# Kernel tuning notes

Hardware: AMD Instinct MI355X
Metric: run time of the kernel (lower is better)

The kernel has to match this reference:

```python
import jax, jax.numpy as jnp
import numpy as np

N, E = 20000, 640000
LATENT, HID, OUT, HEADS = 512, 256, 128, 2
NEG_SLOPE = 0.2


def setup_inputs() -> dict:
    key = jax.random.key(0)
    ks = jax.random.split(key, 12)
    s = 0.02
    return {
        "z": jax.random.normal(ks[0], (N, LATENT), dtype=jnp.float32),
        "edge_index": jax.random.randint(ks[1], (2, E), 0, N, dtype=jnp.int64),
        "W1": jax.random.normal(ks[2], (LATENT, HID), dtype=jnp.float32) * s,
        "b1": jnp.zeros((HID,), dtype=jnp.float32),
        "W2": jax.random.normal(ks[3], (HID, HID * HEADS), dtype=jnp.float32) * s,
        "b2": jnp.zeros((HID * HEADS,), dtype=jnp.float32),
        "Wg": jax.random.normal(ks[4], (HID * HEADS, HEADS * OUT), dtype=jnp.float32) * s,
        "att_src": jax.random.normal(ks[5], (HEADS, OUT), dtype=jnp.float32) * s,
        "att_dst": jax.random.normal(ks[6], (HEADS, OUT), dtype=jnp.float32) * s,
        "bias_g": jnp.zeros((HEADS * OUT,), dtype=jnp.float32),
        "W3": jax.random.normal(ks[7], (OUT * HEADS, 512), dtype=jnp.float32) * s,
        "b3": jnp.zeros((512,), dtype=jnp.float32),
    }


def _gat_conv(x, edge_index, Wg, att_src, att_dst, bias_g):
    n = x.shape[0]
    # add self loops (PyG GATConv default add_self_loops=True)
    loops = jnp.tile(jnp.arange(n, dtype=edge_index.dtype)[None, :], (2, 1))
    ei = jnp.concatenate([edge_index, loops], axis=1)
    src, dst = ei[0], ei[1]
    xp = (x @ Wg).reshape(n, HEADS, OUT)          # [N,H,C]
    a_src = jnp.einsum('nhc,hc->nh', xp, att_src)  # [N,H]
    a_dst = jnp.einsum('nhc,hc->nh', xp, att_dst)
    alpha = jax.nn.leaky_relu(a_src[src] + a_dst[dst], NEG_SLOPE)  # [E+N,H]
    amax = jax.ops.segment_max(alpha, dst, num_segments=n)
    alpha = jnp.exp(alpha - amax[dst])
    denom = jax.ops.segment_sum(alpha, dst, num_segments=n)
    alpha = alpha / jnp.maximum(denom[dst], 1e-16)
    msg = xp[src] * alpha[:, :, None]              # [E+N,H,C]
    out = jax.ops.segment_sum(msg, dst, num_segments=n)  # [N,H,C]
    return out.reshape(n, HEADS * OUT) + bias_g


def reference(z, edge_index, W1, b1, W2, b2, Wg, att_src, att_dst, bias_g, W3, b3):
    x = jax.nn.relu(z @ W1 + b1)
    x = jax.nn.relu(x @ W2 + b2)
    x = _gat_conv(x, edge_index, Wg, att_src, att_dst, bias_g)
    return x @ W3 + b3
```

## Files before the change

### kernel.cpp

```cpp
#include <hip/hip_runtime.h>
#include <hip/hip_bf16.h>
#include <float.h>

#define N_NODES 20000
#define LATENT  512
#define HID     256
#define OUT_C   128
#define HEADS   2
#define HC      256
#define NEG_SLOPE 0.2f

typedef _Float16 half8 __attribute__((ext_vector_type(8)));
typedef __attribute__((ext_vector_type(4))) float f32x4;
typedef __attribute__((ext_vector_type(2))) float f32x2;

__device__ __forceinline__ ushort f2h(float v) {
    _Float16 h = (_Float16)v;
    return *(ushort*)&h;
}
__device__ __forceinline__ float h2f(ushort u) {
    _Float16 h = *(_Float16*)&u;
    return (float)h;
}

#if __has_builtin(__builtin_amdgcn_cvt_pk_fp8_f32) && __has_builtin(__builtin_amdgcn_cvt_pk_f32_fp8)
#define FP8_HW 1
#else
#define FP8_HW 0
#endif

__device__ __forceinline__ uint f32_to_e4m3(float v) {
#if FP8_HW
    return (uint)(__builtin_amdgcn_cvt_pk_fp8_f32(v, v, 0, false) & 0xff);
#else
    _Float16 hf = (_Float16)(v * 0.00390625f);
    uint hb = *(ushort*)&hf;
    uint s = (hb >> 8) & 0x80;
    uint mag = hb & 0x7fff;
    mag = (mag + 0x3f + ((mag >> 7) & 1)) >> 7;
    if (mag > 0x7e) mag = 0x7e;
    return s | mag;
#endif
}

__device__ __forceinline__ void gl_lds16(const ushort* g, ushort* l) {
    __builtin_amdgcn_global_load_lds(
        (const __attribute__((address_space(1))) unsigned int*)g,
        (__attribute__((address_space(3))) unsigned int*)l, 16, 0, 0);
}

__global__ __launch_bounds__(512) void fused_mlp(
    const ushort* __restrict__ z16, const ushort* __restrict__ W1T,
    const float* __restrict__ b1, const ushort* __restrict__ W2T,
    const float* __restrict__ b2, const ushort* __restrict__ WgT,
    const float* __restrict__ attS, const float* __restrict__ attD,
    float* __restrict__ aS, float* __restrict__ aD,
    unsigned char* __restrict__ xp8, int M)
{
    __shared__ ushort lds[65536];

    const int t = threadIdx.x;
    const int l = t & 63;
    const int w = t >> 6;
    const int wr = w & 3;
    const int wc = w >> 2;
    const int lm = l & 15;
    const int q  = l >> 4;
    const int q4 = q * 4;
    const int row0 = (int)blockIdx.x * 64;
    const int lr16 = l >> 2;
    const int gsh = (((l & 3) ^ ((l >> 4) & 3)) << 3);
    const int csw = ((q ^ ((lm >> 2) & 3)) << 3);

    constexpr int X1 = 0;
    constexpr int X2 = 16384;
    constexpr int SB = 49152;

    auto p1b = [&](int c) { int b = c % 3; return b == 0 ? SB : b == 1 ? X2 : X2 + 10240; };
    auto p2b = [&](int c) { int b = c % 3; return b == 0 ? SB : b == 1 ? X2 : X2 + 16384; };
    auto p3b = [&](int c) { int b = c % 3; return b == 0 ? SB : b == 1 ? SB + 8192 : X1; };

    auto issue1 = [&](int c) {
        ushort* B = &lds[p1b(c)];
        const int kk = c * 32;
        #pragma unroll
        for (int u = 0; u < 3; ++u) {
            const int ii = w + u * 8;
            if (ii < 20) {
                const ushort* g = (ii < 4)
                    ? z16 + (size_t)(row0 + ii * 16 + lr16) * 512 + kk + gsh
                    : W1T + (size_t)((ii - 4) * 16 + lr16) * 512 + kk + gsh;
                gl_lds16(g, B + ii * 512);
            }
        }
    };
    auto issue2 = [&](int c) {
        ushort* B = &lds[p2b(c)];
        const int kk = c * 32;
        #pragma unroll
        for (int u = 0; u < 4; ++u) {
            const int ii = w + u * 8;
            gl_lds16(W2T + (size_t)(ii * 16 + lr16) * 256 + kk + gsh, B + ii * 512);
        }
    };
    auto issue3 = [&](int c) {
        ushort* B = &lds[p3b(c)];
        const int kk = c * 32;
        #pragma unroll
        for (int u = 0; u < 2; ++u) {
            const int ii = w + u * 8;
            gl_lds16(WgT + (size_t)(ii * 16 + lr16) * 512 + kk + gsh, B + ii * 512);
        }
    };

    auto wait3i = [&](int c, int NC) {
        __builtin_amdgcn_sched_barrier(0);
        if (c + 1 < NC) {
            if (w < 4) asm volatile("s_waitcnt vmcnt(3)" ::: "memory");
            else       asm volatile("s_waitcnt vmcnt(2)" ::: "memory");
        } else         asm volatile("s_waitcnt vmcnt(0)" ::: "memory");
        __builtin_amdgcn_s_barrier();
        __builtin_amdgcn_sched_barrier(0);
    };
    auto wait4 = [&](int c, int NC) {
        __builtin_amdgcn_sched_barrier(0);
        if (c + 1 < NC) asm volatile("s_waitcnt vmcnt(4)" ::: "memory");
        else            asm volatile("s_waitcnt vmcnt(0)" ::: "memory");
        __builtin_amdgcn_s_barrier();
        __builtin_amdgcn_sched_barrier(0);
    };
    auto wait2 = [&](int c, int NC) {
        __builtin_amdgcn_sched_barrier(0);
        if (c + 1 < NC) asm volatile("s_waitcnt vmcnt(2)" ::: "memory");
        else            asm volatile("s_waitcnt vmcnt(0)" ::: "memory");
        __builtin_amdgcn_s_barrier();
        __builtin_amdgcn_sched_barrier(0);
    };

    const f32x4 zf = {0.f, 0.f, 0.f, 0.f};

    f32x4 acc1[8];
    #pragma unroll
    for (int i = 0; i < 8; ++i) acc1[i] = zf;

    issue1(0); issue1(1);
    for (int c = 0; c < 16; ++c) {
        wait3i(c, 16);
        if (c + 2 < 16) issue1(c + 2);
        const ushort* B = &lds[p1b(c)];
        half8 af = *(const half8*)&B[(wr * 16 + lm) * 32 + csw];
        #pragma unroll
        for (int ni = 0; ni < 8; ++ni) {
            half8 bf = *(const half8*)&B[2048 + (wc * 128 + ni * 16 + lm) * 32 + csw];
            acc1[ni] = __builtin_amdgcn_mfma_f32_16x16x32_f16(af, bf, acc1[ni], 0, 0, 0);
        }
    }
    __builtin_amdgcn_s_barrier();
    issue2(0); issue2(1);
    #pragma unroll
    for (int ni = 0; ni < 8; ++ni) {
        const int col = wc * 128 + ni * 16 + lm;
        const float bv = b1[col];
        const int ch = col >> 5, c5 = col & 31;
        #pragma unroll
        for (int r = 0; r < 4; ++r) {
            const int row = wr * 16 + q4 + r;
            const float v = fmaxf(acc1[ni][r] + bv, 0.f);
            lds[X1 + ch * 2048 + row * 32 + (((c5 >> 3) ^ q) << 3) + (c5 & 7)] = f2h(v);
        }
    }
    asm volatile("s_waitcnt lgkmcnt(0)" ::: "memory");
    __builtin_amdgcn_s_barrier();
    __builtin_amdgcn_sched_barrier(0);

    f32x4 acc2[16];
    #pragma unroll
    for (int i = 0; i < 16; ++i) acc2[i] = zf;

    for (int c = 0; c < 8; ++c) {
        wait4(c, 8);
        if (c + 2 < 8) issue2(c + 2);
        const ushort* B = &lds[p2b(c)];
        half8 af = *(const half8*)&lds[X1 + c * 2048 + (wr * 16 + lm) * 32 + csw];
        #pragma unroll
        for (int ni = 0; ni < 16; ++ni) {
            half8 bf = *(const half8*)&B[(wc * 256 + ni * 16 + lm) * 32 + csw];
            acc2[ni] = __builtin_amdgcn_mfma_f32_16x16x32_f16(af, bf, acc2[ni], 0, 0, 0);
        }
    }
    __builtin_amdgcn_s_barrier();
    issue3(0); issue3(1);
    #pragma unroll
    for (int ni = 0; ni < 16; ++ni) {
        const int col = wc * 256 + ni * 16 + lm;
        const float bv = b2[col];
        const int ch = col >> 5, c5 = col & 31;
        #pragma unroll
        for (int r = 0; r < 4; ++r) {
            const int row = wr * 16 + q4 + r;
            const float v = fmaxf(acc2[ni][r] + bv, 0.f);
            lds[X2 + ch * 2048 + row * 32 + (((c5 >> 3) ^ q) << 3) + (c5 & 7)] = f2h(v);
        }
    }
    asm volatile("s_waitcnt lgkmcnt(0)" ::: "memory");
    __builtin_amdgcn_s_barrier();
    __builtin_amdgcn_sched_barrier(0);

    f32x4 acc3[8];
    #pragma unroll
    for (int i = 0; i < 8; ++i) acc3[i] = zf;

    for (int c = 0; c < 16; ++c) {
        wait2(c, 16);
        if (c + 2 < 16) issue3(c + 2);
        const ushort* B = &lds[p3b(c)];
        half8 af = *(const half8*)&lds[X2 + c * 2048 + (wr * 16 + lm) * 32 + csw];
        #pragma unroll
        for (int ni = 0; ni < 8; ++ni) {
            half8 bf = *(const half8*)&B[(wc * 128 + ni * 16 + lm) * 32 + csw];
            acc3[ni] = __builtin_amdgcn_mfma_f32_16x16x32_f16(af, bf, acc3[ni], 0, 0, 0);
        }
    }

    const int h = wc;
    float asv[8], adv[8];
    #pragma unroll
    for (int ni = 0; ni < 8; ++ni) {
        const int col = wc * 128 + ni * 16 + lm;
        asv[ni] = attS[col];
        adv[ni] = attD[col];
    }
    #pragma unroll
    for (int r = 0; r < 4; ++r) {
        const int row = row0 + wr * 16 + q4 + r;
        float ps = 0.f, pd = 0.f;
        #pragma unroll
        for (int ni = 0; ni < 8; ++ni) {
            const float v = acc3[ni][r];
            ps += v * asv[ni];
            pd += v * adv[ni];
            if (row < M)
                xp8[(size_t)row * HC + wc * 128 + ni * 16 + lm] =
                    (unsigned char)f32_to_e4m3(v);
        }
        #pragma unroll
        for (int off = 8; off > 0; off >>= 1) {
            ps += __shfl_xor(ps, off);
            pd += __shfl_xor(pd, off);
        }
        if (lm == 0 && row < M) {
            atomicAdd(&aS[2 * row + h], ps);
            atomicAdd(&aD[2 * row + h], pd);
        }
    }
}

template<int BN, int LOGNBY>
__global__ __launch_bounds__(256, 4) void gemm_f16(
    const ushort* __restrict__ A, const ushort* __restrict__ BT,
    const float* __restrict__ bias,
    float* __restrict__ Cf, ushort* __restrict__ Ch,
    int M, int N, int K, int relu)
{
    static_assert(BN == 64, "vmcnt immediates assume 3 DMAs/chunk");
    constexpr int NI  = BN / 32;
    constexpr int BUF = 4096 + BN * 32;
    __shared__ ushort lds[3 * BUF];

    const int t = threadIdx.x;
    const int l = t & 63;
    const int w = t >> 6;
    const int wm = (w >> 1) * 64;
    const int wn = (w & 1) * (BN / 2);
    const int lm = l & 15;
    const int q  = l >> 4;
    const int q4 = q * 4;

    const int T  = (int)gridDim.x;
    const int qq = T >> 3, rr = T & 7;
    const int kx = (int)blockIdx.x & 7;
    const int jx = (int)blockIdx.x >> 3;
    const int lin = kx * qq + (kx < rr ? kx : rr) + jx;
    const int row0 = (lin >> LOGNBY) * 128;
    const int col0 = (lin & ((1 << LOGNBY) - 1)) * BN;

    const int jr0 = w * 16 + (l >> 2);
    const int gsh = (((l & 3) ^ ((l >> 4) & 3)) << 3);
    const ushort* gA0 = A + (size_t)(row0 + jr0) * K + gsh;
    const ushort* gA1 = gA0 + (size_t)64 * K;
    const ushort* gB0 = BT + (size_t)(col0 + jr0) * K + gsh;
    const int dA0 = w * 512, dA1 = (4 + w) * 512;
    const int dB0 = 4096 + w * 512;

    const int csw = ((q ^ ((lm >> 2) & 3)) << 3);

    const f32x4 zf = {0.f, 0.f, 0.f, 0.f};
    f32x4 acc[4][NI];
    #pragma unroll
    for (int i = 0; i < 4; ++i)
        #pragma unroll
        for (int j = 0; j < NI; ++j) acc[i][j] = zf;

    const int NC = K >> 5;

    auto issue = [&](int c) {
        ushort* B = lds + (size_t)(c % 3) * BUF;
        const int kk = c * 32;
        gl_lds16(gA0 + kk, B + dA0);
        gl_lds16(gA1 + kk, B + dA1);
        gl_lds16(gB0 + kk, B + dB0);
    };

    auto compute = [&](int c) {
        const ushort* B = lds + (size_t)(c % 3) * BUF;
        half8 bf[NI];
        #pragma unroll
        for (int ni = 0; ni < NI; ++ni) {
            const int boff = (wn + ni * 16 + lm) * 32 + csw;
            bf[ni] = *(const half8*)&B[4096 + boff];
        }
        #pragma unroll
        for (int mi = 0; mi < 4; ++mi) {
            const int aoff = (wm + mi * 16 + lm) * 32 + csw;
            half8 af = *(const half8*)&B[aoff];
            #pragma unroll
            for (int ni = 0; ni < NI; ++ni)
                acc[mi][ni] = __builtin_amdgcn_mfma_f32_16x16x32_f16(
                    af, bf[ni], acc[mi][ni], 0, 0, 0);
        }
    };

    issue(0); issue(1);
    for (int c = 0; c < NC; ++c) {
        __builtin_amdgcn_sched_barrier(0);
        if (c + 1 < NC) asm volatile("s_waitcnt vmcnt(3)" ::: "memory");
        else            asm volatile("s_waitcnt vmcnt(0)" ::: "memory");
        __builtin_amdgcn_s_barrier();
        __builtin_amdgcn_sched_barrier(0);
        if (c + 2 < NC) issue(c + 2);
        compute(c);
    }

    #pragma unroll
    for (int mi = 0; mi < 4; ++mi) {
        #pragma unroll
        for (int ni = 0; ni < NI; ++ni) {
            const int col = col0 + wn + ni * 16 + lm;
            const float bv = bias ? bias[col] : 0.f;
            #pragma unroll
            for (int r = 0; r < 4; ++r) {
                const int row = row0 + wm + mi * 16 + q4 + r;
                if (row >= M) continue;
                float v = acc[mi][ni][r] + bv;
                if (relu) v = fmaxf(v, 0.f);
                const size_t idx = (size_t)row * N + col;
                if (Cf) Cf[idx] = v;
                if (Ch) Ch[idx] = f2h(v);
            }
        }
    }
}

#define CVT_BLOCKS 10000
#define TR_BLOCKS  2048
__global__ __launch_bounds__(256) void prologue_kernel(
    const float* __restrict__ z, ushort* __restrict__ z_f16,
    int* deg, int* cursor, float* aS, float* aD, int n,
    const float* __restrict__ W1, const float* __restrict__ W2,
    const float* __restrict__ Wg, const float* __restrict__ W3,
    ushort* __restrict__ T1, ushort* __restrict__ T2,
    ushort* __restrict__ Tg, ushort* __restrict__ T3)
{
    const int b = blockIdx.x;
    if (b < CVT_BLOCKS) {
        int i = b * 256 + threadIdx.x;
        if (i < n) {
            deg[i] = 0; cursor[i] = 0;
            ((float2*)aS)[i] = make_float2(0.f, 0.f);
            ((float2*)aD)[i] = make_float2(0.f, 0.f);
        }
        float4 v = ((const float4*)z)[i];
        ((ushort4*)z_f16)[i] = make_ushort4(f2h(v.x), f2h(v.y), f2h(v.z), f2h(v.w));
    } else {
        int idx = (b - CVT_BLOCKS) * 256 + threadIdx.x;
        int which = idx >> 17, i = idx & 131071;
        const float* W; ushort* T; int K, N;
        if (which == 0)      { W = W1; T = T1; K = 512; N = 256; }
        else if (which == 1) { W = W2; T = T2; K = 256; N = 512; }
        else if (which == 2) { W = Wg; T = Tg; K = 512; N = 256; }
        else                 { W = W3; T = T3; K = 256; N = 512; }
        int k = i / N, nn = i - k * N;
        T[(size_t)nn * K + k] = f2h(W[i]);
    }
}

__global__ __launch_bounds__(256) void hist_kernel(
    const int* __restrict__ dst, int* deg, int E_real, int ET)
{
    int e = blockIdx.x * blockDim.x + threadIdx.x;
    if (e >= ET) return;
    int d = (e < E_real) ? dst[e] : (e - E_real);
    atomicAdd(&deg[d], 1);
}

__global__ __launch_bounds__(1024) void scan_kernel(
    const int* __restrict__ deg, int* __restrict__ rowptr, int n)
{
    __shared__ int part[1024];
    const int t = threadIdx.x;
    const int chunk = (n + 1023) / 1024;
    const int lo = t * chunk;
    const int hi = min(lo + chunk, n);
    int s = 0;
    for (int i = lo; i < hi; ++i) s += deg[i];
    part[t] = s;
    __syncthreads();
    #pragma unroll
    for (int off = 1; off < 1024; off <<= 1) {
        int add = (t >= off) ? part[t - off] : 0;
        __syncthreads();
        part[t] += add;
        __syncthreads();
    }
    int run = part[t] - s;
    for (int i = lo; i < hi; ++i) { rowptr[i] = run; run += deg[i]; }
    if (t == 1023) rowptr[n] = part[1023];
}

__global__ __launch_bounds__(256) void scatter_kernel(
    const int* __restrict__ src, const int* __restrict__ dst,
    const int* __restrict__ rowptr, int* cursor,
    int* __restrict__ sorted_src, int E_real, int ET)
{
    int e = blockIdx.x * blockDim.x + threadIdx.x;
    if (e >= ET) return;
    int s, d;
    if (e < E_real) { s = src[e]; d = dst[e]; }
    else            { s = e - E_real; d = s; }
    int pos = rowptr[d] + atomicAdd(&cursor[d], 1);
    sorted_src[pos] = s;
}

__global__ __launch_bounds__(256) void gat_aggregate(
    const int* __restrict__ rowptr, const int* __restrict__ sorted_src,
    const float* __restrict__ a_src, const float* __restrict__ a_dst,
    const unsigned char* __restrict__ xp8, const float* __restrict__ bias_g,
    ushort* __restrict__ xg, int n)
{
    const int d = blockIdx.x * 4 + (threadIdx.x >> 6);
    if (d >= n) return;
    const int lane = threadIdx.x & 63;
    const int hsel = lane & 32;
    const int start = rowptr[d], end = rowptr[d + 1];

    const float ad0 = a_dst[2 * d + 0];
    const float ad1 = a_dst[2 * d + 1];

    float4 acc = make_float4(0.f, 0.f, 0.f, 0.f);
    float denom = 0.f;

    for (int e0 = start; e0 < end; e0 += 32) {
        const int cnt = min(32, end - e0);
        const int idx = lane & 31;
        float wsel = 0.f; int off = 0;
        if (idx < cnt) {
            int s = sorted_src[e0 + idx];
            float v0 = a_src[2 * s + 0] + ad0;
            float v1 = a_src[2 * s + 1] + ad1;
            v0 = (v0 > 0.f) ? v0 : NEG_SLOPE * v0;
            v1 = (v1 > 0.f) ? v1 : NEG_SLOPE * v1;
            wsel = (lane < 32) ? __expf(v0) : __expf(v1);
            off = s * HC;
        }
        int j = 0;
        for (; j + 8 <= cnt; j += 8) {
            float w_[8]; int o_[8];
            #pragma unroll
            for (int u = 0; u < 8; ++u) {
                w_[u] = __shfl(wsel, (j + u) + hsel);
                o_[u] = __shfl(off, j + u);
            }
            uint v_[8];
            #pragma unroll
            for (int u = 0; u < 8; ++u)
                v_[u] = *(const uint*)(xp8 + o_[u] + 4 * lane);
            #pragma unroll
            for (int u = 0; u < 8; ++u) {
                denom += w_[u];
#if FP8_HW
                f32x2 lo = __builtin_amdgcn_cvt_pk_f32_fp8((int)v_[u], false);
                f32x2 hi = __builtin_amdgcn_cvt_pk_f32_fp8((int)v_[u], true);
                acc.x += w_[u] * lo.x; acc.y += w_[u] * lo.y;
                acc.z += w_[u] * hi.x; acc.w += w_[u] * hi.y;
#else
                const float wu = w_[u] * 256.0f;
                const uint b = v_[u];
                acc.x += wu * h2f(((b & 0x80u) << 8) | ((b & 0x7fu) << 7));
                acc.y += wu * h2f((((b >> 8) & 0x80u) << 8) | (((b >> 8) & 0x7fu) << 7));
                acc.z += wu * h2f((((b >> 16) & 0x80u) << 8) | (((b >> 16) & 0x7fu) << 7));
                acc.w += wu * h2f((((b >> 24) & 0x80u) << 8) | (((b >> 24) & 0x7fu) << 7));
#endif
            }
        }
        for (; j < cnt; ++j) {
            const float w = __shfl(wsel, j + hsel);
            const int   o = __shfl(off, j);
            const uint  b = *(const uint*)(xp8 + o + 4 * lane);
            denom += w;
#if FP8_HW
            f32x2 lo = __builtin_amdgcn_cvt_pk_f32_fp8((int)b, false);
            f32x2 hi = __builtin_amdgcn_cvt_pk_f32_fp8((int)b, true);
            acc.x += w * lo.x; acc.y += w * lo.y;
            acc.z += w * hi.x; acc.w += w * hi.y;
#else
            const float wu = w * 256.0f;
            acc.x += wu * h2f(((b & 0x80u) << 8) | ((b & 0x7fu) << 7));
            acc.y += wu * h2f((((b >> 8) & 0x80u) << 8) | (((b >> 8) & 0x7fu) << 7));
            acc.z += wu * h2f((((b >> 16) & 0x80u) << 8) | (((b >> 16) & 0x7fu) << 7));
            acc.w += wu * h2f((((b >> 24) & 0x80u) << 8) | (((b >> 24) & 0x7fu) << 7));
#endif
        }
    }

    const float inv = 1.f / fmaxf(denom, 1e-16f);
    const int c = 4 * lane;
    const float4 bg = *(const float4*)(bias_g + c);
    const size_t base = ((size_t)d * HC + c) >> 2;
    ((ushort4*)xg)[base] = make_ushort4(
        f2h(acc.x * inv + bg.x), f2h(acc.y * inv + bg.y),
        f2h(acc.z * inv + bg.z), f2h(acc.w * inv + bg.w));
}

extern "C" void kernel_launch(void* const* d_in, const int* in_sizes, int n_in,
                              void* d_out, int out_size, void* d_ws, size_t ws_size,
                              hipStream_t stream)
{
    const float* z       = (const float*)d_in[0];
    const int*   ei      = (const int*)d_in[1];
    const float* W1      = (const float*)d_in[2];
    const float* b1      = (const float*)d_in[3];
    const float* W2      = (const float*)d_in[4];
    const float* b2      = (const float*)d_in[5];
    const float* Wg      = (const float*)d_in[6];
    const float* att_src = (const float*)d_in[7];
    const float* att_dst = (const float*)d_in[8];
    const float* bias_g  = (const float*)d_in[9];
    const float* W3      = (const float*)d_in[10];
    const float* b3      = (const float*)d_in[11];
    float* out = (float*)d_out;

    const int n = N_NODES;
    const int E_real = in_sizes[1] / 2;
    const int ET = E_real + n;
    const int* src = ei;
    const int* dst = ei + E_real;

    char* p = (char*)d_ws;
    auto alloc = [&](size_t bytes) {
        char* r = p;
        p += (bytes + 63) & ~(size_t)63;
        return r;
    };
    const int np = n + 128;
    ushort* z_f16  = (ushort*)alloc((size_t)np * LATENT * 2);
    ushort* xg_f16 = (ushort*)alloc((size_t)np * HID * 2);
    unsigned char* xp8 = (unsigned char*)alloc((size_t)n * HC);
    ushort* W1T = (ushort*)alloc((size_t)LATENT * HID * 2);
    ushort* W2T = (ushort*)alloc((size_t)HID * 512 * 2);
    ushort* WgT = (ushort*)alloc((size_t)512 * HC * 2);
    ushort* W3T = (ushort*)alloc((size_t)HC * 512 * 2);
    float* a_src = (float*)alloc((size_t)2 * n * 4);
    float* a_dst = (float*)alloc((size_t)2 * n * 4);
    int* deg        = (int*)alloc((size_t)n * 4);
    int* rowptr     = (int*)alloc(((size_t)n + 1) * 4);
    int* cursor     = (int*)alloc((size_t)n * 4);
    int* sorted_src = (int*)alloc((size_t)ET * 4);

    const int gm128 = (n + 127) / 128;

    prologue_kernel<<<CVT_BLOCKS + TR_BLOCKS, 256, 0, stream>>>(
        z, z_f16, deg, cursor, a_src, a_dst, n,
        W1, W2, Wg, W3, W1T, W2T, WgT, W3T);
    hist_kernel<<<(ET + 255) / 256, 256, 0, stream>>>(dst, deg, E_real, ET);
    scan_kernel<<<1, 1024, 0, stream>>>(deg, rowptr, n);
    scatter_kernel<<<(ET + 255) / 256, 256, 0, stream>>>(
        src, dst, rowptr, cursor, sorted_src, E_real, ET);

    fused_mlp<<<(n + 63) / 64, 512, 0, stream>>>(
        z_f16, W1T, b1, W2T, b2, WgT,
        att_src, att_dst, a_src, a_dst, xp8, n);

    gat_aggregate<<<(n + 3) / 4, 256, 0, stream>>>(
        rowptr, sorted_src, a_src, a_dst, xp8, bias_g, xg_f16, n);

    gemm_f16<64, 3><<<gm128 * 8, 256, 0, stream>>>(
        xg_f16, W3T, b3, out, nullptr, n, 512, HC, 0);
}
```

Measured before the change: 296.5 us.

## Slab-stream layer-2 output into layer-3 GEMM to cut LDS and registers

Restructures the fused MLP so the second GEMM is computed in four 128-column slabs, each immediately consumed by the Wg GEMM as a K-chunk, instead of materializing the full 512-wide hidden activation in LDS. This shrinks LDS from 128KB to 80KB and the layer-2 accumulators from 16 to 4 fragments, and adds a launch-bounds occupancy hint of 4. The aim is more resident blocks per CU and better latency hiding. In exchange it adds more barriers, smaller double-buffered loads, and finer-grained waitcnt scheduling, which raises the risk of pipeline stalls.

```diff
diff --git a/kernel.cpp b/kernel.cpp
--- a/kernel.cpp
+++ b/kernel.cpp
@@ -49,7 +49,7 @@
         (__attribute__((address_space(3))) unsigned int*)l, 16, 0, 0);
 }
 
-__global__ __launch_bounds__(512) void fused_mlp(
+__global__ __launch_bounds__(512, 4) void fused_mlp(
     const ushort* __restrict__ z16, const ushort* __restrict__ W1T,
     const float* __restrict__ b1, const ushort* __restrict__ W2T,
     const float* __restrict__ b2, const ushort* __restrict__ WgT,
@@ -57,7 +57,7 @@
     float* __restrict__ aS, float* __restrict__ aD,
     unsigned char* __restrict__ xp8, int M)
 {
-    __shared__ ushort lds[65536];
+    __shared__ ushort lds[40960];
 
     const int t = threadIdx.x;
     const int l = t & 63;
@@ -72,16 +72,17 @@
     const int gsh = (((l & 3) ^ ((l >> 4) & 3)) << 3);
     const int csw = ((q ^ ((lm >> 2) & 3)) << 3);
 
-    constexpr int X1 = 0;
-    constexpr int X2 = 16384;
-    constexpr int SB = 49152;
-
-    auto p1b = [&](int c) { int b = c % 3; return b == 0 ? SB : b == 1 ? X2 : X2 + 10240; };
-    auto p2b = [&](int c) { int b = c % 3; return b == 0 ? SB : b == 1 ? X2 : X2 + 16384; };
-    auto p3b = [&](int c) { int b = c % 3; return b == 0 ? SB : b == 1 ? SB + 8192 : X1; };
+    constexpr int X1   = 0;
+    constexpr int SLAB = 16384;
+    constexpr int SB   = 24576;
+
+    auto barsync = [&]() {
+        __builtin_amdgcn_s_barrier();
+        __builtin_amdgcn_sched_barrier(0);
+    };
 
     auto issue1 = [&](int c) {
-        ushort* B = &lds[p1b(c)];
+        ushort* B = &lds[(c % 3) * 10240];
         const int kk = c * 32;
         #pragma unroll
         for (int u = 0; u < 3; ++u) {
@@ -94,60 +95,37 @@
             }
         }
     };
-    auto issue2 = [&](int c) {
-        ushort* B = &lds[p2b(c)];
-        const int kk = c * 32;
-        #pragma unroll
-        for (int u = 0; u < 4; ++u) {
-            const int ii = w + u * 8;
-            gl_lds16(W2T + (size_t)(ii * 16 + lr16) * 256 + kk + gsh, B + ii * 512);
-        }
-    };
-    auto issue3 = [&](int c) {
-        ushort* B = &lds[p3b(c)];
-        const int kk = c * 32;
+    auto issue2 = [&](int s, int c) {
+        ushort* B = &lds[SLAB + (c & 1) * 4096];
+        gl_lds16(W2T + (size_t)(s * 128 + w * 16 + lr16) * 256 + c * 32 + gsh,
+                 B + w * 512);
+    };
+    auto issue3 = [&](int s, int c) {
+        ushort* B = &lds[SB + (c & 1) * 8192];
         #pragma unroll
         for (int u = 0; u < 2; ++u) {
             const int ii = w + u * 8;
-            gl_lds16(WgT + (size_t)(ii * 16 + lr16) * 512 + kk + gsh, B + ii * 512);
-        }
-    };
-
-    auto wait3i = [&](int c, int NC) {
+            gl_lds16(WgT + (size_t)(ii * 16 + lr16) * 512 + s * 128 + c * 32 + gsh,
+                     B + ii * 512);
+        }
+    };
+
+    const f32x4 zf = {0.f, 0.f, 0.f, 0.f};
+
+    f32x4 acc1[8];
+    #pragma unroll
+    for (int i = 0; i < 8; ++i) acc1[i] = zf;
+
+    issue1(0); issue1(1);
+    for (int c = 0; c < 16; ++c) {
         __builtin_amdgcn_sched_barrier(0);
-        if (c + 1 < NC) {
+        if (c + 1 < 16) {
             if (w < 4) asm volatile("s_waitcnt vmcnt(3)" ::: "memory");
             else       asm volatile("s_waitcnt vmcnt(2)" ::: "memory");
         } else         asm volatile("s_waitcnt vmcnt(0)" ::: "memory");
-        __builtin_amdgcn_s_barrier();
-        __builtin_amdgcn_sched_barrier(0);
-    };
-    auto wait4 = [&](int c, int NC) {
-        __builtin_amdgcn_sched_barrier(0);
-        if (c + 1 < NC) asm volatile("s_waitcnt vmcnt(4)" ::: "memory");
-        else            asm volatile("s_waitcnt vmcnt(0)" ::: "memory");
-        __builtin_amdgcn_s_barrier();
-        __builtin_amdgcn_sched_barrier(0);
-    };
-    auto wait2 = [&](int c, int NC) {
-        __builtin_amdgcn_sched_barrier(0);
-        if (c + 1 < NC) asm volatile("s_waitcnt vmcnt(2)" ::: "memory");
-        else            asm volatile("s_waitcnt vmcnt(0)" ::: "memory");
-        __builtin_amdgcn_s_barrier();
-        __builtin_amdgcn_sched_barrier(0);
-    };
-
-    const f32x4 zf = {0.f, 0.f, 0.f, 0.f};
-
-    f32x4 acc1[8];
-    #pragma unroll
-    for (int i = 0; i < 8; ++i) acc1[i] = zf;
-
-    issue1(0); issue1(1);
-    for (int c = 0; c < 16; ++c) {
-        wait3i(c, 16);
+        barsync();
         if (c + 2 < 16) issue1(c + 2);
-        const ushort* B = &lds[p1b(c)];
+        const ushort* B = &lds[(c % 3) * 10240];
         half8 af = *(const half8*)&B[(wr * 16 + lm) * 32 + csw];
         #pragma unroll
         for (int ni = 0; ni < 8; ++ni) {
@@ -156,7 +134,7 @@
         }
     }
     __builtin_amdgcn_s_barrier();
-    issue2(0); issue2(1);
+    issue2(0, 0); issue2(0, 1);
     #pragma unroll
     for (int ni = 0; ni < 8; ++ni) {
         const int col = wc * 128 + ni * 16 + lm;
@@ -170,56 +148,68 @@
         }
     }
     asm volatile("s_waitcnt lgkmcnt(0)" ::: "memory");
-    __builtin_amdgcn_s_barrier();
-    __builtin_amdgcn_sched_barrier(0);
-
-    f32x4 acc2[16];
-    #pragma unroll
-    for (int i = 0; i < 16; ++i) acc2[i] = zf;
-
-    for (int c = 0; c < 8; ++c) {
-        wait4(c, 8);
-        if (c + 2 < 8) issue2(c + 2);
-        const ushort* B = &lds[p2b(c)];
-        half8 af = *(const half8*)&lds[X1 + c * 2048 + (wr * 16 + lm) * 32 + csw];
-        #pragma unroll
-        for (int ni = 0; ni < 16; ++ni) {
-            half8 bf = *(const half8*)&B[(wc * 256 + ni * 16 + lm) * 32 + csw];
-            acc2[ni] = __builtin_amdgcn_mfma_f32_16x16x32_f16(af, bf, acc2[ni], 0, 0, 0);
-        }
-    }
-    __builtin_amdgcn_s_barrier();
-    issue3(0); issue3(1);
-    #pragma unroll
-    for (int ni = 0; ni < 16; ++ni) {
-        const int col = wc * 256 + ni * 16 + lm;
-        const float bv = b2[col];
-        const int ch = col >> 5, c5 = col & 31;
-        #pragma unroll
-        for (int r = 0; r < 4; ++r) {
-            const int row = wr * 16 + q4 + r;
-            const float v = fmaxf(acc2[ni][r] + bv, 0.f);
-            lds[X2 + ch * 2048 + row * 32 + (((c5 >> 3) ^ q) << 3) + (c5 & 7)] = f2h(v);
-        }
-    }
-    asm volatile("s_waitcnt lgkmcnt(0)" ::: "memory");
-    __builtin_amdgcn_s_barrier();
-    __builtin_amdgcn_sched_barrier(0);
+    barsync();
 
     f32x4 acc3[8];
     #pragma unroll
     for (int i = 0; i < 8; ++i) acc3[i] = zf;
 
-    for (int c = 0; c < 16; ++c) {
-        wait2(c, 16);
-        if (c + 2 < 16) issue3(c + 2);
-        const ushort* B = &lds[p3b(c)];
-        half8 af = *(const half8*)&lds[X2 + c * 2048 + (wr * 16 + lm) * 32 + csw];
-        #pragma unroll
-        for (int ni = 0; ni < 8; ++ni) {
-            half8 bf = *(const half8*)&B[(wc * 128 + ni * 16 + lm) * 32 + csw];
-            acc3[ni] = __builtin_amdgcn_mfma_f32_16x16x32_f16(af, bf, acc3[ni], 0, 0, 0);
-        }
+    for (int s = 0; s < 4; ++s) {
+        f32x4 acc2[4];
+        #pragma unroll
+        for (int i = 0; i < 4; ++i) acc2[i] = zf;
+
+        for (int c = 0; c < 8; ++c) {
+            __builtin_amdgcn_sched_barrier(0);
+            if (c == 0) asm volatile("s_waitcnt vmcnt(1)" ::: "memory");
+            else        asm volatile("s_waitcnt vmcnt(0)" ::: "memory");
+            barsync();
+            if (c >= 1 && c + 1 < 8) issue2(s, c + 1);
+            if (c == 7) { issue3(s, 0); issue3(s, 1); }
+            const ushort* Bf = &lds[SLAB + (c & 1) * 4096];
+            half8 af = *(const half8*)&lds[X1 + c * 2048 + (wr * 16 + lm) * 32 + csw];
+            #pragma unroll
+            for (int ni = 0; ni < 4; ++ni) {
+                half8 bf = *(const half8*)&Bf[(wc * 64 + ni * 16 + lm) * 32 + csw];
+                acc2[ni] = __builtin_amdgcn_mfma_f32_16x16x32_f16(af, bf, acc2[ni], 0, 0, 0);
+            }
+        }
+        __builtin_amdgcn_s_barrier();
+        #pragma unroll
+        for (int ni = 0; ni < 4; ++ni) {
+            const int c7 = wc * 64 + ni * 16 + lm;
+            const float bv = b2[s * 128 + c7];
+            const int ch = c7 >> 5, c5 = c7 & 31;
+            #pragma unroll
+            for (int r = 0; r < 4; ++r) {
+                const int row = wr * 16 + q4 + r;
+                const float v = fmaxf(acc2[ni][r] + bv, 0.f);
+                lds[SLAB + ch * 2048 + row * 32 + (((c5 >> 3) ^ q) << 3) + (c5 & 7)] = f2h(v);
+            }
+        }
+        asm volatile("s_waitcnt lgkmcnt(0)" ::: "memory");
+        barsync();
+
+        for (int c = 0; c < 4; ++c) {
+            __builtin_amdgcn_sched_barrier(0);
+            if (c == 0)                asm volatile("s_waitcnt vmcnt(2)" ::: "memory");
+            else if (c == 3 && s < 3)  asm volatile("s_waitcnt vmcnt(1)" ::: "memory");
+            else                       asm volatile("s_waitcnt vmcnt(0)" ::: "memory");
+            barsync();
+            if (c == 1) issue3(s, 2);
+            if (c == 2) { issue3(s, 3);
+                          if (s < 3) issue2(s + 1, 0); }
+            const ushort* Bf = &lds[SB + (c & 1) * 8192];
+            half8 af = *(const half8*)&lds[SLAB + c * 2048 + (wr * 16 + lm) * 32 + csw];
+            #pragma unroll
+            for (int ni = 0; ni < 8; ++ni) {
+                half8 bf = *(const half8*)&Bf[(wc * 128 + ni * 16 + lm) * 32 + csw];
+                acc3[ni] = __builtin_amdgcn_mfma_f32_16x16x32_f16(af, bf, acc3[ni], 0, 0, 0);
+            }
+        }
+        __builtin_amdgcn_s_barrier();
+        if (s < 3) issue2(s + 1, 1);
+        __builtin_amdgcn_sched_barrier(0);
     }
 
     const int h = wc;
```

After: 289.1 us. 2.5% less time.
